# Optimization experiments

Measured on AMD Instinct MI355X. Metric: run time of the kernel, lower is better.

## Reference

```python
import jax, jax.numpy as jnp
import numpy as np


def _spectral_norm(W, u):
    # W: [out, in] (1x1 conv weight flattened), u: [out]
    # one power-iteration step (torch does this under no_grad), then
    # sigma = u' @ W @ v with gradient flowing through W only.
    v = W.T @ u
    v = v / jnp.linalg.norm(v)
    u2 = W @ v
    u2 = u2 / jnp.linalg.norm(u2)
    v = jax.lax.stop_gradient(v)
    u2 = jax.lax.stop_gradient(u2)
    sigma = u2 @ (W @ v)
    return W / sigma


def setup_inputs() -> dict:
    key = jax.random.key(0)
    ks = jax.random.split(key, 8)
    B, C, H, W = 32, 512, 32, 32
    Cq = C // 8  # 64
    x = jax.random.normal(ks[0], (B, C, H, W), dtype=jnp.float32)
    s = 1.0 / np.sqrt(C)
    return {
        "x": x,
        "Wq": jax.random.normal(ks[1], (Cq, C), dtype=jnp.float32) * s,
        "bq": jnp.zeros((Cq,), dtype=jnp.float32),
        "uq": jax.random.normal(ks[2], (Cq,), dtype=jnp.float32),
        "Wk": jax.random.normal(ks[3], (Cq, C), dtype=jnp.float32) * s,
        "bk": jnp.zeros((Cq,), dtype=jnp.float32),
        "uk": jax.random.normal(ks[4], (Cq,), dtype=jnp.float32),
        "Wv": jax.random.normal(ks[5], (C, C), dtype=jnp.float32) * s,
        "bv": jnp.zeros((C,), dtype=jnp.float32),
        "uv": jax.random.normal(ks[6], (C,), dtype=jnp.float32),
        "gamma": jnp.float32(0.5),
    }


def reference(x, Wq, bq, uq, Wk, bk, uk, Wv, bv, uv, gamma):
    B, C, H, W = x.shape
    N = H * W
    f = x.reshape(B, C, N)                                   # [B,C,N]
    # 1x1 conv == channel matmul with spectral-normalized weights
    q = jnp.einsum('oc,bcn->bno', _spectral_norm(Wq, uq), f) + bq          # [B,N,Cq]
    k = jnp.einsum('oc,bcn->bon', _spectral_norm(Wk, uk), f) + bk[:, None]  # [B,Cq,N]
    v = jnp.einsum('oc,bcn->bon', _spectral_norm(Wv, uv), f) + bv[:, None]  # [B,C,N]
    qk = jnp.einsum('bno,bom->bnm', q, k)                    # [B,N,N], no 1/sqrt(d)
    attn = jax.nn.softmax(qk, axis=1)                        # softmax over QUERY axis (dim 1)
    o = jnp.einsum('bcn,bnm->bcm', v, attn).reshape(B, C, H, W)
    return gamma * o + x
```

## Files before the change

### kernel.cpp

```cpp
#include <hip/hip_runtime.h>
#include <hip/hip_bf16.h>

typedef __hip_bfloat16 bf16;
typedef __bf16 bf16x8 __attribute__((ext_vector_type(8)));
typedef float  f32x4  __attribute__((ext_vector_type(4)));
typedef unsigned short u16x8 __attribute__((ext_vector_type(8)));

#define C_IN  512
#define N_SP  1024
#define BATCH 32

__device__ __forceinline__ float ldmix(const void* p, size_t i, int f32) {
    return f32 ? ((const float*)p)[i] : __bfloat162float(((const bf16*)p)[i]);
}
__device__ __forceinline__ void stmix(void* p, size_t i, float v, int f32) {
    if (f32) ((float*)p)[i] = v;
    else     ((bf16*)p)[i] = __float2bfloat16(v);
}
__device__ __forceinline__ unsigned short bfbits(float f) {
    bf16 t = __float2bfloat16(f);
    return *reinterpret_cast<unsigned short*>(&t);
}
__device__ __forceinline__ float bf2f(unsigned short h) {
    union { unsigned u; float f; } c; c.u = ((unsigned)h) << 16; return c.f;
}
__device__ __forceinline__ void ldvec8(const void* W, size_t base, int f32, float v[8]) {
    if (f32) {
        const float4* p = reinterpret_cast<const float4*>((const float*)W + base);
        float4 a = p[0], b = p[1];
        v[0] = a.x; v[1] = a.y; v[2] = a.z; v[3] = a.w;
        v[4] = b.x; v[5] = b.y; v[6] = b.z; v[7] = b.w;
    } else {
        u16x8 h = *reinterpret_cast<const u16x8*>((const bf16*)W + base);
#pragma unroll
        for (int j = 0; j < 8; ++j) v[j] = bf2f(h[j]);
    }
}

__device__ __forceinline__ void gload_lds16(const bf16* g, void* l) {
    __builtin_amdgcn_global_load_lds(
        (__attribute__((address_space(1))) void*)(g),
        (__attribute__((address_space(3))) void*)(l),
        16, 0, 0);
}

#define STAGE64(LDS, GROW, GPITCH, K0) do {                                    \
    int _c = (wave << 6) + lane; int _r = _c >> 2;                             \
    int _s = (_c & 3) ^ ((_r >> 1) & 3);                                       \
    gload_lds16((GROW) + (size_t)_r * (GPITCH) + (K0) + _s * 8,                \
                (char*)(LDS) + (wave << 10));                                  \
} while (0)

__device__ __forceinline__ bf16x8 swz_frag(const void* tile, int row, int quad) {
    return *(const bf16x8*)((const char*)tile + (row << 6) +
                            ((quad ^ ((row >> 1) & 3)) << 4));
}

#define STGUNIT(SLOT, AROW, APITCH, BROW, BPITCH, KOFF) do {                   \
    char* _ub = lds + (size_t)(SLOT) * 32768;                                  \
    _Pragma("unroll")                                                          \
    for (int _i = 0; _i < 2; ++_i) {                                           \
        int _c = ((wave * 2 + _i) << 6) + lane;                                \
        int _r = _c >> 2; int _s = (_c & 3) ^ ((_r >> 1) & 3);                 \
        gload_lds16((AROW) + (size_t)_r * (APITCH) + (KOFF) + _s * 8,          \
                    _ub + ((wave * 2 + _i) << 10));                            \
    }                                                                          \
    _Pragma("unroll")                                                          \
    for (int _i = 0; _i < 2; ++_i) {                                           \
        int _c = ((wave * 2 + _i) << 6) + lane;                                \
        int _r = _c >> 2; int _s = (_c & 3) ^ ((_r >> 1) & 3);                 \
        gload_lds16((BROW) + (size_t)_r * (BPITCH) + (KOFF) + _s * 8,          \
                    _ub + 16384 + ((wave * 2 + _i) << 10));                    \
    }                                                                          \
} while (0)

__device__ __forceinline__ bf16x8 frag32(const char* part, int row, int quad) {
    return *(const bf16x8*)(part + (row << 6) +
                            ((quad ^ ((row >> 1) & 3)) << 4));
}

#define WAIT4_BARRIER() do {                                                   \
    asm volatile("s_waitcnt vmcnt(4)" ::: "memory");                           \
    __builtin_amdgcn_sched_barrier(0);                                         \
    __builtin_amdgcn_s_barrier();                                              \
    __builtin_amdgcn_sched_barrier(0);                                         \
} while (0)

__device__ __forceinline__ void tile_decode(int bid, int nblk, int& z, int& mc) {
    int GBk = nblk >> 5;
    if ((GBk & 7) == 0) {
        z  = (bid & 7) + 8 * ((bid >> 3) >> 5);
        mc = (bid >> 3) & 31;
    } else {
        z  = bid >> 5;
        mc = bid & 31;
    }
}
__device__ __forceinline__ void tile_decode8(int bid, int nblk, int& z, int& mc) {
    int GBk = nblk >> 3;
    if ((GBk & 7) == 0) {
        z  = (bid & 7) + 8 * (bid >> 6);
        mc = (bid >> 3) & 7;
    } else {
        z  = bid >> 3;
        mc = bid & 7;
    }
}

__global__ void k_detect(const unsigned short* __restrict__ xh, int* __restrict__ flag)
{
    __shared__ int red[256];
    int tid = threadIdx.x;
    unsigned short h = xh[2 * tid];
    int e = (h >> 7) & 0xFF;
    red[tid] = (e == 0 || (e >= 96 && e <= 159)) ? 1 : 0;
    __syncthreads();
    for (int s = 128; s > 0; s >>= 1) { if (tid < s) red[tid] += red[tid + s]; __syncthreads(); }
    if (tid == 0) *flag = (red[0] < 192) ? 1 : 0;
}

__global__ __launch_bounds__(256) void k_sn1(
    const void* __restrict__ Wq, const void* __restrict__ uq,
    const void* __restrict__ Wk, const void* __restrict__ uk,
    const void* __restrict__ Wv, const void* __restrict__ uv,
    const int* __restrict__ flag, float* __restrict__ tpart)
{
    __shared__ float sh_u[64];
    __shared__ float sh_acc[4][512];
    int f32 = *flag;
    int bx = blockIdx.x;
    const void *W, *u; int oc, slot;
    if (bx == 0)      { W = Wq; u = uq; oc = 0;      slot = 0; }
    else if (bx == 1) { W = Wk; u = uk; oc = 0;      slot = 1; }
    else              { W = Wv; u = uv; oc = bx - 2; slot = bx; }
    int tid = threadIdx.x, wave = tid >> 6, lane = tid & 63;
    if (tid < 64) sh_u[tid] = ldmix(u, oc * 64 + tid, f32);
    __syncthreads();

    float acc[8];
#pragma unroll
    for (int j = 0; j < 8; ++j) acc[j] = 0.f;
    int obase = oc * 64 + wave * 16;
#pragma unroll 4
    for (int i = 0; i < 16; ++i) {
        int o = obase + i;
        float w8[8]; ldvec8(W, (size_t)o * C_IN + lane * 8, f32, w8);
        float uo = sh_u[o - oc * 64];
#pragma unroll
        for (int j = 0; j < 8; ++j) acc[j] += w8[j] * uo;
    }
#pragma unroll
    for (int j = 0; j < 8; ++j) sh_acc[wave][lane * 8 + j] = acc[j];
    __syncthreads();
    for (int c = tid; c < 512; c += 256)
        tpart[(size_t)slot * 512 + c] =
            sh_acc[0][c] + sh_acc[1][c] + sh_acc[2][c] + sh_acc[3][c];
}

__global__ __launch_bounds__(512) void k_sn2(
    const void* __restrict__ Wq, const void* __restrict__ Wk,
    const void* __restrict__ Wv, const int* __restrict__ flag,
    const float* __restrict__ tpart, float* __restrict__ sig)
{
    __shared__ float sh_t[512];
    __shared__ float red[512];
    int f32 = *flag;
    int m = blockIdx.x;
    const void* W; int out, slot0, nch;
    if (m == 0)      { W = Wq; out = 64;  slot0 = 0; nch = 1; }
    else if (m == 1) { W = Wk; out = 64;  slot0 = 1; nch = 1; }
    else             { W = Wv; out = 512; slot0 = 2; nch = 8; }
    int tid = threadIdx.x, wave = tid >> 6, lane = tid & 63;

    float t = 0.f;
    for (int c2 = 0; c2 < nch; ++c2) t += tpart[(size_t)(slot0 + c2) * 512 + tid];
    sh_t[tid] = t;
    red[tid] = t * t;
    __syncthreads();
    for (int s = 256; s > 0; s >>= 1) { if (tid < s) red[tid] += red[tid + s]; __syncthreads(); }
    float t2 = red[0];
    __syncthreads();

    float tl[8];
#pragma unroll
    for (int j = 0; j < 8; ++j) tl[j] = sh_t[lane * 8 + j];

    float s2 = 0.f;
#pragma unroll 2
    for (int o = wave; o < out; o += 8) {
        float w8[8]; ldvec8(W, (size_t)o * C_IN + lane * 8, f32, w8);
        float d = 0.f;
#pragma unroll
        for (int j = 0; j < 8; ++j) d += w8[j] * tl[j];
#pragma unroll
        for (int off = 32; off > 0; off >>= 1) d += __shfl_xor(d, off);
        if (lane == 0) s2 += d * d;
    }
    __syncthreads();
    red[tid] = (lane == 0) ? s2 : 0.f;
    __syncthreads();
    for (int s = 256; s > 0; s >>= 1) { if (tid < s) red[tid] += red[tid + s]; __syncthreads(); }
    if (tid == 0) sig[m] = sqrtf(t2 / red[0]);
}

__global__ __launch_bounds__(256) void k_wscale(
    const void* __restrict__ Wq, const void* __restrict__ bq,
    const void* __restrict__ Wk, const void* __restrict__ bk,
    const void* __restrict__ Wv, const void* __restrict__ bv,
    const float* __restrict__ sig, const int* __restrict__ flag,
    bf16* __restrict__ Wb, bf16* __restrict__ Wlo, float* __restrict__ biasf)
{
    int f32 = *flag;
    int r = blockIdx.x;
    const void *W, *b; int row; float s;
    if (r < 64)       { W = Wq; b = bq; row = r;       s = sig[0]; }
    else if (r < 128) { W = Wk; b = bk; row = r - 64;  s = sig[1]; }
    else              { W = Wv; b = bv; row = r - 128; s = sig[2]; }
    for (int c = threadIdx.x; c < C_IN; c += 256) {
        float w = ldmix(W, (size_t)row * C_IN + c, f32) * s;
        bf16 hi = __float2bfloat16(w);
        Wb[(size_t)r * C_IN + c] = hi;
        if (r < 128)
            Wlo[(size_t)r * C_IN + c] = __float2bfloat16(w - __bfloat162float(hi));
    }
    if (threadIdx.x == 0) biasf[r] = ldmix(b, row, f32);
}

__global__ __launch_bounds__(256) void k_xt(
    const void* __restrict__ x, const int* __restrict__ flag,
    char* __restrict__ SX, int batch0)
{
    __shared__ float tile[64][65];
    int f32 = *flag;
    int z = blockIdx.z;
    int n0 = blockIdx.x * 64, c0 = blockIdx.y * 64;
    size_t xoff = (size_t)(batch0 + z) * C_IN * N_SP;
    bf16* xTh = (bf16*)(SX + (size_t)z * 4194304);
    bf16* xTl = xTh + 524288;
    int tid = threadIdx.x;
#pragma unroll
    for (int i = 0; i < 4; ++i) {
        int idx = tid + i * 256;
        int c = idx >> 4, nq = idx & 15;
#pragma unroll
        for (int t = 0; t < 4; ++t)
            tile[c][nq * 4 + t] = ldmix(x, xoff + (size_t)(c0 + c) * N_SP + n0 + nq * 4 + t, f32);
    }
    __syncthreads();
#pragma unroll
    for (int i = 0; i < 16; ++i) {
        int idx = tid + i * 256;
        int n = idx >> 6, c = idx & 63;
        float v = tile[c][n];
        bf16 hi = __float2bfloat16(v);
        xTh[(size_t)(n0 + n) * C_IN + c0 + c] = hi;
        xTl[(size_t)(n0 + n) * C_IN + c0 + c] = __float2bfloat16(v - __bfloat162float(hi));
    }
}

__global__ __launch_bounds__(512, 1) void k_qkv_v(
    const bf16* __restrict__ Wb, const float* __restrict__ biasf,
    const char* __restrict__ SX, bf16* __restrict__ YV)
{
    extern __shared__ char lds[];
    int z, mc; tile_decode8(blockIdx.x, gridDim.x, z, mc);
    int r0 = 128 + (mc >> 2) * 256;
    int n0 = (mc & 3) * 256;
    const bf16* xTh = (const bf16*)(SX + (size_t)z * 4194304);
    bf16* Yv = YV + (size_t)z * 524288;
    int tid = threadIdx.x, wave = tid >> 6, lane = tid & 63, quad = lane >> 4, l16 = lane & 15;
    int wr = wave >> 2, wc4 = wave & 3;

    const bf16* Ar = Wb + (size_t)r0 * C_IN;
    const bf16* Br = xTh + (size_t)n0 * C_IN;

    f32x4 acc[8][4];
#pragma unroll
    for (int i = 0; i < 8; ++i)
#pragma unroll
        for (int j = 0; j < 4; ++j) acc[i][j] = (f32x4){0.f, 0.f, 0.f, 0.f};

    STGUNIT(0, Ar, C_IN, Br, C_IN, 0);
    STGUNIT(1, Ar, C_IN, Br, C_IN, 32);

    const int NT = 8;
    for (int t = 0; t < NT; ++t) {
        int d = t & 1;
#pragma unroll
        for (int kh = 0; kh < 2; ++kh) {
            const char* unit = lds + (size_t)(d * 2 + kh) * 32768;
            WAIT4_BARRIER();
            if (t + 1 < NT)
                STGUNIT((d ^ 1) * 2 + kh, Ar, C_IN, Br, C_IN, (t + 1) * 64 + kh * 32);
            bf16x8 bfr[4];
#pragma unroll
            for (int fn = 0; fn < 4; ++fn)
                bfr[fn] = frag32(unit + 16384, wc4 * 64 + fn * 16 + l16, quad);
            bf16x8 af[4];
#pragma unroll
            for (int fm = 0; fm < 4; ++fm)
                af[fm] = frag32(unit, wr * 128 + fm * 16 + l16, quad);
            __builtin_amdgcn_s_setprio(1);
#pragma unroll
            for (int fm = 0; fm < 4; ++fm)
#pragma unroll
                for (int fn = 0; fn < 4; ++fn)
                    acc[fm][fn] = __builtin_amdgcn_mfma_f32_16x16x32_bf16(af[fm], bfr[fn], acc[fm][fn], 0, 0, 0);
            __builtin_amdgcn_s_setprio(0);
#pragma unroll
            for (int fm = 0; fm < 4; ++fm)
                af[fm] = frag32(unit, wr * 128 + (fm + 4) * 16 + l16, quad);
            __builtin_amdgcn_s_setprio(1);
#pragma unroll
            for (int fm = 0; fm < 4; ++fm)
#pragma unroll
                for (int fn = 0; fn < 4; ++fn)
                    acc[fm + 4][fn] = __builtin_amdgcn_mfma_f32_16x16x32_bf16(af[fm], bfr[fn], acc[fm + 4][fn], 0, 0, 0);
            __builtin_amdgcn_s_setprio(0);
        }
    }

#pragma unroll
    for (int fm = 0; fm < 8; ++fm)
#pragma unroll
        for (int fn = 0; fn < 4; ++fn)
#pragma unroll
            for (int r = 0; r < 4; ++r) {
                int c = r0 + wr * 128 + fm * 16 + quad * 4 + r;
                int n = n0 + wc4 * 64 + fn * 16 + l16;
                Yv[(size_t)(c - 128) * N_SP + n] = __float2bfloat16(acc[fm][fn][r] + biasf[c]);
            }
}

__global__ __launch_bounds__(256) void k_qkv_qk(
    const bf16* __restrict__ Wb, const bf16* __restrict__ Wlo,
    const float* __restrict__ biasf, const char* __restrict__ SX,
    bf16* __restrict__ QT, bf16* __restrict__ KT)
{
    __shared__ __bf16 Ah_[3][64][32], Al_[3][64][32], Bh_[3][64][32], Bl_[3][64][32];
    int z, mc; tile_decode(blockIdx.x, gridDim.x, z, mc);
    int n0 = (mc >> 1) * 64;
    int m0 = (mc & 1) * 64;
    const bf16* xTh = (const bf16*)(SX + (size_t)z * 4194304);
    const bf16* xTl = xTh + 524288;
    bf16* qt = QT + (size_t)z * 65536;
    bf16* kt = KT + (size_t)z * 65536;
    int tid = threadIdx.x, wave = tid >> 6, lane = tid & 63, quad = lane >> 4, l16 = lane & 15;
    int wmh = (wave >> 1) * 32, wnh = (wave & 1) * 32;

    const bf16* Ahr = Wb  + (size_t)m0 * C_IN;
    const bf16* Alr = Wlo + (size_t)m0 * C_IN;
    const bf16* Bhr = xTh + (size_t)n0 * C_IN;
    const bf16* Blr = xTl + (size_t)n0 * C_IN;

    f32x4 acc[2][2];
#pragma unroll
    for (int i = 0; i < 2; ++i)
#pragma unroll
        for (int j = 0; j < 2; ++j) acc[i][j] = (f32x4){0.f, 0.f, 0.f, 0.f};

    STAGE64(Ah_[0], Ahr, C_IN, 0);  STAGE64(Al_[0], Alr, C_IN, 0);
    STAGE64(Bh_[0], Bhr, C_IN, 0);  STAGE64(Bl_[0], Blr, C_IN, 0);
    STAGE64(Ah_[1], Ahr, C_IN, 32); STAGE64(Al_[1], Alr, C_IN, 32);
    STAGE64(Bh_[1], Bhr, C_IN, 32); STAGE64(Bl_[1], Blr, C_IN, 32);
    char *ah0 = (char*)Ah_[0], *ah1 = (char*)Ah_[1], *ah2 = (char*)Ah_[2];
    char *al0 = (char*)Al_[0], *al1 = (char*)Al_[1], *al2 = (char*)Al_[2];
    char *bh0 = (char*)Bh_[0], *bh1 = (char*)Bh_[1], *bh2 = (char*)Bh_[2];
    char *bl0 = (char*)Bl_[0], *bl1 = (char*)Bl_[1], *bl2 = (char*)Bl_[2];

#define QK_MFMA(PAH, PAL, PBH, PBL) {                                          \
    bf16x8 fah[2], fal[2], fbh[2], fbl[2];                                     \
    _Pragma("unroll")                                                          \
    for (int i = 0; i < 2; ++i) {                                              \
        fah[i] = swz_frag(PAH, wmh + i * 16 + l16, quad);                      \
        fal[i] = swz_frag(PAL, wmh + i * 16 + l16, quad);                      \
    }                                                                          \
    _Pragma("unroll")                                                          \
    for (int j = 0; j < 2; ++j) {                                              \
        fbh[j] = swz_frag(PBH, wnh + j * 16 + l16, quad);                      \
        fbl[j] = swz_frag(PBL, wnh + j * 16 + l16, quad);                      \
    }                                                                          \
    __builtin_amdgcn_s_setprio(1);                                             \
    _Pragma("unroll")                                                          \
    for (int i = 0; i < 2; ++i)                                                \
        _Pragma("unroll")                                                      \
        for (int j = 0; j < 2; ++j) {                                          \
            acc[i][j] = __builtin_amdgcn_mfma_f32_16x16x32_bf16(fah[i], fbh[j], acc[i][j], 0, 0, 0); \
            acc[i][j] = __builtin_amdgcn_mfma_f32_16x16x32_bf16(fah[i], fbl[j], acc[i][j], 0, 0, 0); \
            acc[i][j] = __builtin_amdgcn_mfma_f32_16x16x32_bf16(fal[i], fbh[j], acc[i][j], 0, 0, 0); \
        }                                                                      \
    __builtin_amdgcn_s_setprio(0); }

    for (int t = 0; t < 15; ++t) {
        asm volatile("s_waitcnt vmcnt(4)" ::: "memory");
        __builtin_amdgcn_s_barrier();
        __builtin_amdgcn_sched_barrier(0);
        if (t + 2 < 16) {
            int k2 = (t + 2) * 32;
            STAGE64(ah2, Ahr, C_IN, k2); STAGE64(al2, Alr, C_IN, k2);
            STAGE64(bh2, Bhr, C_IN, k2); STAGE64(bl2, Blr, C_IN, k2);
        }
        QK_MFMA(ah0, al0, bh0, bl0);
        char* tp = ah0; ah0 = ah1; ah1 = ah2; ah2 = tp;
        tp = al0; al0 = al1; al1 = al2; al2 = tp;
        tp = bh0; bh0 = bh1; bh1 = bh2; bh2 = tp;
        tp = bl0; bl0 = bl1; bl1 = bl2; bl2 = tp;
    }
    asm volatile("s_waitcnt vmcnt(0)" ::: "memory");
    __builtin_amdgcn_s_barrier();
    __builtin_amdgcn_sched_barrier(0);
    QK_MFMA(ah0, al0, bh0, bl0);
#undef QK_MFMA

#pragma unroll
    for (int i = 0; i < 2; ++i)
#pragma unroll
        for (int j = 0; j < 2; ++j) {
            int cbase = m0 + wmh + i * 16 + quad * 4;
            int n = n0 + wnh + j * 16 + l16;
            ushort4 st;
            st.x = bfbits(acc[i][j][0] + biasf[cbase + 0]);
            st.y = bfbits(acc[i][j][1] + biasf[cbase + 1]);
            st.z = bfbits(acc[i][j][2] + biasf[cbase + 2]);
            st.w = bfbits(acc[i][j][3] + biasf[cbase + 3]);
            bf16* dst = (m0 == 0) ? &qt[(size_t)n * 64 + cbase]
                                  : &kt[(size_t)n * 64 + (cbase - 64)];
            *reinterpret_cast<ushort4*>(dst) = st;
        }
}

__global__ __launch_bounds__(256) void k_qk(
    const bf16* __restrict__ QT, const bf16* __restrict__ KT,
    char* __restrict__ SX)
{
    __shared__ __bf16 Als[128][40];
    __shared__ __bf16 Bls[128][40];
    int z = blockIdx.z, m0 = blockIdx.y * 128, n0 = blockIdx.x * 128;
    const bf16* qt = QT + (size_t)z * 65536;
    const bf16* kt = KT + (size_t)z * 65536;
    float* Sf = (float*)(SX + (size_t)z * 4194304);
    int tid = threadIdx.x, wave = tid >> 6, lane = tid & 63, quad = lane >> 4, l16 = lane & 15;
    int wc = (wave >> 1) * 64, wm = (wave & 1) * 64;

    f32x4 acc[4][4];
#pragma unroll
    for (int i = 0; i < 4; ++i)
#pragma unroll
        for (int j = 0; j < 4; ++j) acc[i][j] = (f32x4){0.f, 0.f, 0.f, 0.f};

#pragma unroll
    for (int k0 = 0; k0 < 64; k0 += 32) {
#pragma unroll
        for (int s = 0; s < 2; ++s) {
            int idx = tid + s * 256; int row = idx >> 2, ch = idx & 3;
            *reinterpret_cast<uint4*>(&Als[row][ch * 8]) =
                *reinterpret_cast<const uint4*>(&kt[(size_t)(m0 + row) * 64 + k0 + ch * 8]);
            *reinterpret_cast<uint4*>(&Bls[row][ch * 8]) =
                *reinterpret_cast<const uint4*>(&qt[(size_t)(n0 + row) * 64 + k0 + ch * 8]);
        }
        __syncthreads();
        bf16x8 a[4], b[4];
#pragma unroll
        for (int i = 0; i < 4; ++i)
            a[i] = *reinterpret_cast<const bf16x8*>(&Als[wc + i * 16 + l16][quad * 8]);
#pragma unroll
        for (int j = 0; j < 4; ++j)
            b[j] = *reinterpret_cast<const bf16x8*>(&Bls[wm + j * 16 + l16][quad * 8]);
#pragma unroll
        for (int i = 0; i < 4; ++i)
#pragma unroll
            for (int j = 0; j < 4; ++j)
                acc[i][j] = __builtin_amdgcn_mfma_f32_16x16x32_bf16(a[i], b[j], acc[i][j], 0, 0, 0);
        __syncthreads();
    }
#pragma unroll
    for (int i = 0; i < 4; ++i)
#pragma unroll
        for (int j = 0; j < 4; ++j)
#pragma unroll
            for (int r = 0; r < 4; ++r) {
                int m = m0 + wc + i * 16 + quad * 4 + r;
                int n = n0 + wm + j * 16 + l16;
                Sf[(size_t)m * N_SP + n] = acc[i][j][r];
            }
}

__global__ __launch_bounds__(256) void k_softmax(char* __restrict__ SX)
{
    __shared__ float red[256];
    int z = blockIdx.x >> 10, m = blockIdx.x & 1023;
    float* p = (float*)(SX + (size_t)z * 4194304) + (size_t)m * N_SP;
    bf16* pb = (bf16*)p;
    int tid = threadIdx.x;
    float v0 = p[tid], v1 = p[tid + 256], v2 = p[tid + 512], v3 = p[tid + 768];
    red[tid] = fmaxf(fmaxf(v0, v1), fmaxf(v2, v3));
    __syncthreads();
    for (int s = 128; s > 0; s >>= 1) { if (tid < s) red[tid] = fmaxf(red[tid], red[tid + s]); __syncthreads(); }
    float mx = red[0];
    __syncthreads();
    float d0 = fmaxf(fminf(v0 - mx, 0.f), -80.f);
    float d1 = fmaxf(fminf(v1 - mx, 0.f), -80.f);
    float d2 = fmaxf(fminf(v2 - mx, 0.f), -80.f);
    float d3 = fmaxf(fminf(v3 - mx, 0.f), -80.f);
    float e0 = __expf(d0), e1 = __expf(d1), e2 = __expf(d2), e3 = __expf(d3);
    red[tid] = e0 + e1 + e2 + e3;
    __syncthreads();
    for (int s = 128; s > 0; s >>= 1) { if (tid < s) red[tid] += red[tid + s]; __syncthreads(); }
    float inv = 1.f / red[0];
    pb[tid]       = __float2bfloat16(e0 * inv);
    pb[tid + 256] = __float2bfloat16(e1 * inv);
    pb[tid + 512] = __float2bfloat16(e2 * inv);
    pb[tid + 768] = __float2bfloat16(e3 * inv);
}

__global__ __launch_bounds__(512, 1) void k_out(
    const bf16* __restrict__ YV, const char* __restrict__ SX,
    const void* __restrict__ x, const void* __restrict__ gamma,
    const int* __restrict__ flag, void* __restrict__ out, int batch0)
{
    extern __shared__ char lds[];
    int f32 = *flag;
    int z, mc; tile_decode8(blockIdx.x, gridDim.x, z, mc);
    int c0 = (mc >> 2) * 256;
    int m0 = (mc & 3) * 256;
    const bf16* Yv = YV + (size_t)z * 524288;
    const bf16* Pb = (const bf16*)(SX + (size_t)z * 4194304);
    int tid = threadIdx.x, wave = tid >> 6, lane = tid & 63, quad = lane >> 4, l16 = lane & 15;
    int wr = wave >> 2, wc4 = wave & 3;

    const bf16* Ar = Yv + (size_t)c0 * N_SP;
    const bf16* Br = Pb + (size_t)m0 * 2048;

    f32x4 acc[8][4];
#pragma unroll
    for (int i = 0; i < 8; ++i)
#pragma unroll
        for (int j = 0; j < 4; ++j) acc[i][j] = (f32x4){0.f, 0.f, 0.f, 0.f};

    STGUNIT(0, Ar, N_SP, Br, 2048, 0);
    STGUNIT(1, Ar, N_SP, Br, 2048, 32);

    const int NT = 16;
    for (int t = 0; t < NT; ++t) {
        int d = t & 1;
#pragma unroll
        for (int kh = 0; kh < 2; ++kh) {
            const char* unit = lds + (size_t)(d * 2 + kh) * 32768;
            WAIT4_BARRIER();
            if (t + 1 < NT)
                STGUNIT((d ^ 1) * 2 + kh, Ar, N_SP, Br, 2048, (t + 1) * 64 + kh * 32);
            bf16x8 bfr[4];
#pragma unroll
            for (int fn = 0; fn < 4; ++fn)
                bfr[fn] = frag32(unit + 16384, wc4 * 64 + fn * 16 + l16, quad);
            bf16x8 af[4];
#pragma unroll
            for (int fm = 0; fm < 4; ++fm)
                af[fm] = frag32(unit, wr * 128 + fm * 16 + l16, quad);
            __builtin_amdgcn_s_setprio(1);
#pragma unroll
            for (int fm = 0; fm < 4; ++fm)
#pragma unroll
                for (int fn = 0; fn < 4; ++fn)
                    acc[fm][fn] = __builtin_amdgcn_mfma_f32_16x16x32_bf16(af[fm], bfr[fn], acc[fm][fn], 0, 0, 0);
            __builtin_amdgcn_s_setprio(0);
#pragma unroll
            for (int fm = 0; fm < 4; ++fm)
                af[fm] = frag32(unit, wr * 128 + (fm + 4) * 16 + l16, quad);
            __builtin_amdgcn_s_setprio(1);
#pragma unroll
            for (int fm = 0; fm < 4; ++fm)
#pragma unroll
                for (int fn = 0; fn < 4; ++fn)
                    acc[fm + 4][fn] = __builtin_amdgcn_mfma_f32_16x16x32_bf16(af[fm], bfr[fn], acc[fm + 4][fn], 0, 0, 0);
            __builtin_amdgcn_s_setprio(0);
        }
    }

    float g = ldmix(gamma, 0, f32);
    const size_t base = (size_t)(batch0 + z) * C_IN * N_SP;
#pragma unroll
    for (int fm = 0; fm < 8; ++fm)
#pragma unroll
        for (int fn = 0; fn < 4; ++fn)
#pragma unroll
            for (int r = 0; r < 4; ++r) {
                int c = c0 + wr * 128 + fm * 16 + quad * 4 + r;
                int m = m0 + wc4 * 64 + fn * 16 + l16;
                size_t o = base + (size_t)c * N_SP + m;
                float v = fmaf(g, acc[fm][fn][r], ldmix(x, o, f32));
                if (!(v == v)) v = 5555.0f + 1000.0f * f32;
                stmix(out, o, v, f32);
            }
}

__global__ void k_wsfail(float* __restrict__ out, int n)
{
    int i = blockIdx.x * 256 + threadIdx.x;
    if (i < n) out[i] = 7777.0f;
}

extern "C" void kernel_launch(void* const* d_in, const int* in_sizes, int n_in,
                              void* d_out, int out_size, void* d_ws, size_t ws_size,
                              hipStream_t stream)
{
    const void* x  = d_in[0];
    const void* Wq = d_in[1];
    const void* bq = d_in[2];
    const void* Wk = d_in[4];
    const void* bk = d_in[5];
    const void* Wv = d_in[7];
    const void* bv = d_in[8];
    const void* uq = d_in[3];
    const void* uk = d_in[6];
    const void* uv = d_in[9];
    const void* gm = d_in[10];

    static int lds_opt_done = 0;
    if (!lds_opt_done) {
        (void)hipFuncSetAttribute(reinterpret_cast<const void*>(k_qkv_v),
                                  hipFuncAttributeMaxDynamicSharedMemorySize, 131072);
        (void)hipFuncSetAttribute(reinterpret_cast<const void*>(k_out),
                                  hipFuncAttributeMaxDynamicSharedMemorySize, 131072);
        lds_opt_done = 1;
    }

    const size_t HDR = 790528;
    const size_t per = 4194304 + 131072 + 131072 + 1048576;
    int GB = 0;
    for (int g = 32; g >= 1; g >>= 1)
        if (HDR + (size_t)g * per <= ws_size) { GB = g; break; }
    if (GB == 0) {
        k_wsfail<<<(out_size + 255) / 256, 256, 0, stream>>>((float*)d_out, out_size);
        return;
    }
    char* ws = (char*)d_ws;
    int*   flag  = (int*)ws;
    float* sig   = (float*)(ws + 16);
    float* biasf = (float*)(ws + 256);
    bf16*  Wb    = (bf16*)(ws + 4096);
    bf16*  Wlo   = (bf16*)(ws + 659456);
    char*  SX    = ws + HDR;
    bf16*  QT    = (bf16*)(SX + (size_t)GB * 4194304);
    bf16*  KT    = QT + (size_t)GB * 65536;
    bf16*  YV    = KT + (size_t)GB * 65536;
    float* tpart = (float*)SX;

    k_detect<<<1, 256, 0, stream>>>((const unsigned short*)x, flag);
    k_sn1<<<10, 256, 0, stream>>>(Wq, uq, Wk, uk, Wv, uv, flag, tpart);
    k_sn2<<<3, 512, 0, stream>>>(Wq, Wk, Wv, flag, tpart, sig);
    k_wscale<<<640, 256, 0, stream>>>(Wq, bq, Wk, bk, Wv, bv, sig, flag, Wb, Wlo, biasf);
    for (int b0 = 0; b0 < BATCH; b0 += GB) {
        k_xt     <<<dim3(16, 8, GB), 256, 0, stream>>>(x, flag, SX, b0);
        k_qkv_v  <<<GB * 8, 512, 131072, stream>>>(Wb, biasf, SX, YV);
        k_qkv_qk <<<GB * 32, 256, 0, stream>>>(Wb, Wlo, biasf, SX, QT, KT);
        k_qk     <<<dim3(8, 8, GB), 256, 0, stream>>>(QT, KT, SX);
        k_softmax<<<GB * 1024, 256, 0, stream>>>(SX);
        k_out    <<<GB * 8, 512, 131072, stream>>>(YV, SX, x, gm, flag, d_out, b0);
    }
}
```

Before: 396.7 us.

## Halve GEMM M-tile and use triple-buffered K=32 pipeline in V and output GEMMs

```diff
diff --git a/kernel.cpp b/kernel.cpp
--- a/kernel.cpp
+++ b/kernel.cpp
@@ -56,21 +56,17 @@
                             ((quad ^ ((row >> 1) & 3)) << 4));
 }
 
-#define STGUNIT(SLOT, AROW, APITCH, BROW, BPITCH, KOFF) do {                   \
-    char* _ub = lds + (size_t)(SLOT) * 32768;                                  \
+#define STGU(UB, AROW, APITCH, BROW, BPITCH, KOFF) do {                        \
+    { int _c = (wave << 6) + lane; int _r = _c >> 2;                           \
+      int _s = (_c & 3) ^ ((_r >> 1) & 3);                                     \
+      gload_lds16((AROW) + (size_t)_r * (APITCH) + (KOFF) + _s * 8,            \
+                  (char*)(UB) + (wave << 10)); }                               \
     _Pragma("unroll")                                                          \
     for (int _i = 0; _i < 2; ++_i) {                                           \
-        int _c = ((wave * 2 + _i) << 6) + lane;                                \
-        int _r = _c >> 2; int _s = (_c & 3) ^ ((_r >> 1) & 3);                 \
-        gload_lds16((AROW) + (size_t)_r * (APITCH) + (KOFF) + _s * 8,          \
-                    _ub + ((wave * 2 + _i) << 10));                            \
-    }                                                                          \
-    _Pragma("unroll")                                                          \
-    for (int _i = 0; _i < 2; ++_i) {                                           \
-        int _c = ((wave * 2 + _i) << 6) + lane;                                \
-        int _r = _c >> 2; int _s = (_c & 3) ^ ((_r >> 1) & 3);                 \
+        int _c = ((wave * 2 + _i) << 6) + lane; int _r = _c >> 2;              \
+        int _s = (_c & 3) ^ ((_r >> 1) & 3);                                   \
         gload_lds16((BROW) + (size_t)_r * (BPITCH) + (KOFF) + _s * 8,          \
-                    _ub + 16384 + ((wave * 2 + _i) << 10));                    \
+                    (char*)(UB) + 8192 + ((wave * 2 + _i) << 10));             \
     }                                                                          \
 } while (0)
 
@@ -79,8 +75,8 @@
                             ((quad ^ ((row >> 1) & 3)) << 4));
 }
 
-#define WAIT4_BARRIER() do {                                                   \
-    asm volatile("s_waitcnt vmcnt(4)" ::: "memory");                           \
+#define WAITN_BARRIER(N) do {                                                  \
+    asm volatile("s_waitcnt vmcnt(" #N ")" ::: "memory");                      \
     __builtin_amdgcn_sched_barrier(0);                                         \
     __builtin_amdgcn_s_barrier();                                              \
     __builtin_amdgcn_sched_barrier(0);                                         \
@@ -96,14 +92,14 @@
         mc = bid & 31;
     }
 }
-__device__ __forceinline__ void tile_decode8(int bid, int nblk, int& z, int& mc) {
-    int GBk = nblk >> 3;
+__device__ __forceinline__ void tile_decode16(int bid, int nblk, int& z, int& mc) {
+    int GBk = nblk >> 4;
     if ((GBk & 7) == 0) {
-        z  = (bid & 7) + 8 * (bid >> 6);
-        mc = (bid >> 3) & 7;
+        z  = (bid & 7) + 8 * (bid >> 7);
+        mc = (bid >> 3) & 15;
     } else {
-        z  = bid >> 3;
-        mc = bid & 7;
+        z  = bid >> 4;
+        mc = bid & 15;
     }
 }
 
@@ -258,13 +254,13 @@
     }
 }
 
-__global__ __launch_bounds__(512, 1) void k_qkv_v(
+__global__ __launch_bounds__(512, 4) void k_qkv_v(
     const bf16* __restrict__ Wb, const float* __restrict__ biasf,
     const char* __restrict__ SX, bf16* __restrict__ YV)
 {
     extern __shared__ char lds[];
-    int z, mc; tile_decode8(blockIdx.x, gridDim.x, z, mc);
-    int r0 = 128 + (mc >> 2) * 256;
+    int z, mc; tile_decode16(blockIdx.x, gridDim.x, z, mc);
+    int r0 = 128 + (mc >> 2) * 128;
     int n0 = (mc & 3) * 256;
     const bf16* xTh = (const bf16*)(SX + (size_t)z * 4194304);
     bf16* Yv = YV + (size_t)z * 524288;
@@ -274,59 +270,53 @@
     const bf16* Ar = Wb + (size_t)r0 * C_IN;
     const bf16* Br = xTh + (size_t)n0 * C_IN;
 
-    f32x4 acc[8][4];
-#pragma unroll
-    for (int i = 0; i < 8; ++i)
+    f32x4 acc[4][4];
+#pragma unroll
+    for (int i = 0; i < 4; ++i)
 #pragma unroll
         for (int j = 0; j < 4; ++j) acc[i][j] = (f32x4){0.f, 0.f, 0.f, 0.f};
 
-    STGUNIT(0, Ar, C_IN, Br, C_IN, 0);
-    STGUNIT(1, Ar, C_IN, Br, C_IN, 32);
-
-    const int NT = 8;
-    for (int t = 0; t < NT; ++t) {
-        int d = t & 1;
-#pragma unroll
-        for (int kh = 0; kh < 2; ++kh) {
-            const char* unit = lds + (size_t)(d * 2 + kh) * 32768;
-            WAIT4_BARRIER();
-            if (t + 1 < NT)
-                STGUNIT((d ^ 1) * 2 + kh, Ar, C_IN, Br, C_IN, (t + 1) * 64 + kh * 32);
-            bf16x8 bfr[4];
-#pragma unroll
-            for (int fn = 0; fn < 4; ++fn)
-                bfr[fn] = frag32(unit + 16384, wc4 * 64 + fn * 16 + l16, quad);
-            bf16x8 af[4];
-#pragma unroll
-            for (int fm = 0; fm < 4; ++fm)
-                af[fm] = frag32(unit, wr * 128 + fm * 16 + l16, quad);
-            __builtin_amdgcn_s_setprio(1);
-#pragma unroll
-            for (int fm = 0; fm < 4; ++fm)
-#pragma unroll
-                for (int fn = 0; fn < 4; ++fn)
-                    acc[fm][fn] = __builtin_amdgcn_mfma_f32_16x16x32_bf16(af[fm], bfr[fn], acc[fm][fn], 0, 0, 0);
-            __builtin_amdgcn_s_setprio(0);
-#pragma unroll
-            for (int fm = 0; fm < 4; ++fm)
-                af[fm] = frag32(unit, wr * 128 + (fm + 4) * 16 + l16, quad);
-            __builtin_amdgcn_s_setprio(1);
-#pragma unroll
-            for (int fm = 0; fm < 4; ++fm)
-#pragma unroll
-                for (int fn = 0; fn < 4; ++fn)
-                    acc[fm + 4][fn] = __builtin_amdgcn_mfma_f32_16x16x32_bf16(af[fm], bfr[fn], acc[fm + 4][fn], 0, 0, 0);
-            __builtin_amdgcn_s_setprio(0);
+    STGU(lds,         Ar, C_IN, Br, C_IN, 0);
+    STGU(lds + 24576, Ar, C_IN, Br, C_IN, 32);
+
+#define VG_MFMA(UB) {                                                          \
+    bf16x8 af[4], bfr[4];                                                      \
+    _Pragma("unroll")                                                          \
+    for (int fm = 0; fm < 4; ++fm)                                             \
+        af[fm] = frag32(UB, wr * 64 + fm * 16 + l16, quad);                    \
+    _Pragma("unroll")                                                          \
+    for (int fn = 0; fn < 4; ++fn)                                             \
+        bfr[fn] = frag32((UB) + 8192, wc4 * 64 + fn * 16 + l16, quad);         \
+    __builtin_amdgcn_s_setprio(1);                                             \
+    _Pragma("unroll")                                                          \
+    for (int fm = 0; fm < 4; ++fm)                                             \
+        _Pragma("unroll")                                                      \
+        for (int fn = 0; fn < 4; ++fn)                                         \
+            acc[fm][fn] = __builtin_amdgcn_mfma_f32_16x16x32_bf16(af[fm], bfr[fn], acc[fm][fn], 0, 0, 0); \
+    __builtin_amdgcn_s_setprio(0); }
+
+    const int NT = 16;
+    int bsel = 0;
+    for (int t = 0; t < NT - 1; ++t) {
+        WAITN_BARRIER(3);
+        if (t + 2 < NT) {
+            int nb = bsel + 2; if (nb >= 3) nb -= 3;
+            STGU(lds + (size_t)nb * 24576, Ar, C_IN, Br, C_IN, (t + 2) * 32);
         }
-    }
-
-#pragma unroll
-    for (int fm = 0; fm < 8; ++fm)
+        VG_MFMA(lds + (size_t)bsel * 24576);
+        if (++bsel == 3) bsel = 0;
+    }
+    WAITN_BARRIER(0);
+    VG_MFMA(lds + (size_t)bsel * 24576);
+#undef VG_MFMA
+
+#pragma unroll
+    for (int fm = 0; fm < 4; ++fm)
 #pragma unroll
         for (int fn = 0; fn < 4; ++fn)
 #pragma unroll
             for (int r = 0; r < 4; ++r) {
-                int c = r0 + wr * 128 + fm * 16 + quad * 4 + r;
+                int c = r0 + wr * 64 + fm * 16 + quad * 4 + r;
                 int n = n0 + wc4 * 64 + fn * 16 + l16;
                 Yv[(size_t)(c - 128) * N_SP + n] = __float2bfloat16(acc[fm][fn][r] + biasf[c]);
             }
@@ -513,15 +503,15 @@
     pb[tid + 768] = __float2bfloat16(e3 * inv);
 }
 
-__global__ __launch_bounds__(512, 1) void k_out(
+__global__ __launch_bounds__(512, 4) void k_out(
     const bf16* __restrict__ YV, const char* __restrict__ SX,
     const void* __restrict__ x, const void* __restrict__ gamma,
     const int* __restrict__ flag, void* __restrict__ out, int batch0)
 {
     extern __shared__ char lds[];
     int f32 = *flag;
-    int z, mc; tile_decode8(blockIdx.x, gridDim.x, z, mc);
-    int c0 = (mc >> 2) * 256;
+    int z, mc; tile_decode16(blockIdx.x, gridDim.x, z, mc);
+    int c0 = (mc >> 2) * 128;
     int m0 = (mc & 3) * 256;
     const bf16* Yv = YV + (size_t)z * 524288;
     const bf16* Pb = (const bf16*)(SX + (size_t)z * 4194304);
@@ -531,61 +521,55 @@
     const bf16* Ar = Yv + (size_t)c0 * N_SP;
     const bf16* Br = Pb + (size_t)m0 * 2048;
 
-    f32x4 acc[8][4];
-#pragma unroll
-    for (int i = 0; i < 8; ++i)
+    f32x4 acc[4][4];
+#pragma unroll
+    for (int i = 0; i < 4; ++i)
 #pragma unroll
         for (int j = 0; j < 4; ++j) acc[i][j] = (f32x4){0.f, 0.f, 0.f, 0.f};
 
-    STGUNIT(0, Ar, N_SP, Br, 2048, 0);
-    STGUNIT(1, Ar, N_SP, Br, 2048, 32);
-
-    const int NT = 16;
-    for (int t = 0; t < NT; ++t) {
-        int d = t & 1;
-#pragma unroll
-        for (int kh = 0; kh < 2; ++kh) {
-            const char* unit = lds + (size_t)(d * 2 + kh) * 32768;
-            WAIT4_BARRIER();
-            if (t + 1 < NT)
-                STGUNIT((d ^ 1) * 2 + kh, Ar, N_SP, Br, 2048, (t + 1) * 64 + kh * 32);
-            bf16x8 bfr[4];
-#pragma unroll
-            for (int fn = 0; fn < 4; ++fn)
-                bfr[fn] = frag32(unit + 16384, wc4 * 64 + fn * 16 + l16, quad);
-            bf16x8 af[4];
-#pragma unroll
-            for (int fm = 0; fm < 4; ++fm)
-                af[fm] = frag32(unit, wr * 128 + fm * 16 + l16, quad);
-            __builtin_amdgcn_s_setprio(1);
-#pragma unroll
-            for (int fm = 0; fm < 4; ++fm)
-#pragma unroll
-                for (int fn = 0; fn < 4; ++fn)
-                    acc[fm][fn] = __builtin_amdgcn_mfma_f32_16x16x32_bf16(af[fm], bfr[fn], acc[fm][fn], 0, 0, 0);
-            __builtin_amdgcn_s_setprio(0);
-#pragma unroll
-            for (int fm = 0; fm < 4; ++fm)
-                af[fm] = frag32(unit, wr * 128 + (fm + 4) * 16 + l16, quad);
-            __builtin_amdgcn_s_setprio(1);
-#pragma unroll
-            for (int fm = 0; fm < 4; ++fm)
-#pragma unroll
-                for (int fn = 0; fn < 4; ++fn)
-                    acc[fm + 4][fn] = __builtin_amdgcn_mfma_f32_16x16x32_bf16(af[fm], bfr[fn], acc[fm + 4][fn], 0, 0, 0);
-            __builtin_amdgcn_s_setprio(0);
+    STGU(lds,         Ar, N_SP, Br, 2048, 0);
+    STGU(lds + 24576, Ar, N_SP, Br, 2048, 32);
+
+#define O_MFMA(UB) {                                                           \
+    bf16x8 af[4], bfr[4];                                                      \
+    _Pragma("unroll")                                                          \
+    for (int fm = 0; fm < 4; ++fm)                                             \
+        af[fm] = frag32(UB, wr * 64 + fm * 16 + l16, quad);                    \
+    _Pragma("unroll")                                                          \
+    for (int fn = 0; fn < 4; ++fn)                                             \
+        bfr[fn] = frag32((UB) + 8192, wc4 * 64 + fn * 16 + l16, quad);         \
+    __builtin_amdgcn_s_setprio(1);                                             \
+    _Pragma("unroll")                                                          \
+    for (int fm = 0; fm < 4; ++fm)                                             \
+        _Pragma("unroll")                                                      \
+        for (int fn = 0; fn < 4; ++fn)                                         \
+            acc[fm][fn] = __builtin_amdgcn_mfma_f32_16x16x32_bf16(af[fm], bfr[fn], acc[fm][fn], 0, 0, 0); \
+    __builtin_amdgcn_s_setprio(0); }
+
+    const int NT = 32;
+    int bsel = 0;
+    for (int t = 0; t < NT - 1; ++t) {
+        WAITN_BARRIER(3);
+        if (t + 2 < NT) {
+            int nb = bsel + 2; if (nb >= 3) nb -= 3;
+            STGU(lds + (size_t)nb * 24576, Ar, N_SP, Br, 2048, (t + 2) * 32);
         }
-    }
+        O_MFMA(lds + (size_t)bsel * 24576);
+        if (++bsel == 3) bsel = 0;
+    }
+    WAITN_BARRIER(0);
+    O_MFMA(lds + (size_t)bsel * 24576);
+#undef O_MFMA
 
     float g = ldmix(gamma, 0, f32);
     const size_t base = (size_t)(batch0 + z) * C_IN * N_SP;
 #pragma unroll
-    for (int fm = 0; fm < 8; ++fm)
+    for (int fm = 0; fm < 4; ++fm)
 #pragma unroll
         for (int fn = 0; fn < 4; ++fn)
 #pragma unroll
             for (int r = 0; r < 4; ++r) {
-                int c = c0 + wr * 128 + fm * 16 + quad * 4 + r;
+                int c = c0 + wr * 64 + fm * 16 + quad * 4 + r;
                 int m = m0 + wc4 * 64 + fn * 16 + l16;
                 size_t o = base + (size_t)c * N_SP + m;
                 float v = fmaf(g, acc[fm][fn][r], ldmix(x, o, f32));
@@ -619,9 +603,9 @@
     static int lds_opt_done = 0;
     if (!lds_opt_done) {
         (void)hipFuncSetAttribute(reinterpret_cast<const void*>(k_qkv_v),
-                                  hipFuncAttributeMaxDynamicSharedMemorySize, 131072);
+                                  hipFuncAttributeMaxDynamicSharedMemorySize, 73728);
         (void)hipFuncSetAttribute(reinterpret_cast<const void*>(k_out),
-                                  hipFuncAttributeMaxDynamicSharedMemorySize, 131072);
+                                  hipFuncAttributeMaxDynamicSharedMemorySize, 73728);
         lds_opt_done = 1;
     }
 
@@ -652,10 +636,10 @@
     k_wscale<<<640, 256, 0, stream>>>(Wq, bq, Wk, bk, Wv, bv, sig, flag, Wb, Wlo, biasf);
     for (int b0 = 0; b0 < BATCH; b0 += GB) {
         k_xt     <<<dim3(16, 8, GB), 256, 0, stream>>>(x, flag, SX, b0);
-        k_qkv_v  <<<GB * 8, 512, 131072, stream>>>(Wb, biasf, SX, YV);
+        k_qkv_v  <<<GB * 16, 512, 73728, stream>>>(Wb, biasf, SX, YV);
         k_qkv_qk <<<GB * 32, 256, 0, stream>>>(Wb, Wlo, biasf, SX, QT, KT);
         k_qk     <<<dim3(8, 8, GB), 256, 0, stream>>>(QT, KT, SX);
         k_softmax<<<GB * 1024, 256, 0, stream>>>(SX);
-        k_out    <<<GB * 8, 512, 131072, stream>>>(YV, SX, x, gm, flag, d_out, b0);
-    }
-}
+        k_out    <<<GB * 16, 512, 73728, stream>>>(YV, SX, x, gm, flag, d_out, b0);
+    }
+}
```

Measured after the change: 387.9 us. 1.02x faster.
